# Kernel tuning notes

Measured on AMD Instinct MI355X. Metric: run time of the kernel, lower is better.

## Reference

```python
import jax, jax.numpy as jnp
import numpy as np

N = 50000          # nodes
E = 800000         # edges
F_IN = 128         # node_features
HID = 128          # hidden_dim
OUT = 64           # out_channels
TOP = 4            # top_features (gate channels)
EXP = 3            # experts
G = 64             # num graphs in batch
TEMP = 101.0       # 100 - 0/(200*0.01) + final_temperature(1.0) at batch counter 0


def setup_inputs() -> dict:
    key = jax.random.key(0)
    ks = jax.random.split(key, 12)
    s = 0.08  # weight init scale
    x = jax.random.normal(ks[0], (N, F_IN), jnp.float32)
    top_features = jax.random.normal(ks[1], (N, TOP), jnp.float32)
    edge_index = jax.random.randint(ks[2], (2, E), 0, N, dtype=jnp.int64)
    batch = jnp.sort(jax.random.randint(ks[3], (N,), 0, G, dtype=jnp.int64))
    W0 = jax.random.normal(ks[4], (EXP, F_IN, HID), jnp.float32) * s
    b0 = jax.random.normal(ks[5], (EXP, HID), jnp.float32) * s
    Wg0 = jax.random.normal(ks[6], (EXP, TOP), jnp.float32) * s
    W1 = jax.random.normal(ks[7], (EXP, HID, HID), jnp.float32) * s
    b1 = jax.random.normal(ks[8], (EXP, HID), jnp.float32) * s
    Wg1 = jax.random.normal(ks[9], (EXP, TOP), jnp.float32) * s
    Wf = jax.random.normal(ks[10], (HID, OUT), jnp.float32) * s
    bf = jax.random.normal(ks[11], (OUT,), jnp.float32) * s
    return {"x": x, "top_features": top_features, "edge_index": edge_index,
            "batch": batch, "W0": W0, "b0": b0, "Wg0": Wg0,
            "W1": W1, "b1": b1, "Wg1": Wg1, "Wf": Wf, "bf": bf}


def reference(x, top_features, edge_index, batch, W0, b0, Wg0, W1, b1, Wg1, Wf, bf):
    # GCN with self-loops and symmetric normalization (PyG GCNConv default)
    sl = jnp.arange(N, dtype=edge_index.dtype)
    src = jnp.concatenate([edge_index[0], sl])
    dst = jnp.concatenate([edge_index[1], sl])
    deg = jax.ops.segment_sum(jnp.ones_like(src, jnp.float32), dst, num_segments=N)
    dinv = jax.lax.rsqrt(deg)  # deg >= 1 thanks to self loops
    norm = dinv[src] * dinv[dst]  # [E+N]

    def camoe_layer(h, W, b, Wg):
        # gate: softmax over experts at temperature TEMP
        gate = jax.nn.softmax((top_features @ Wg.T) / TEMP, axis=-1)  # [N, EXP]
        out = jnp.zeros((N, W.shape[2]), h.dtype)
        for e in range(EXP):  # small fixed expert loop (keeps peak memory low)
            he = h @ W[e]                                            # [N, HID]
            agg = jax.ops.segment_sum(he[src] * norm[:, None], dst, num_segments=N)
            out = out + gate[:, e:e + 1] * jax.nn.relu(agg + b[e])
        return out

    h = camoe_layer(x, W0, b0, Wg0)
    # F.dropout before last layer: eval mode -> identity
    h = camoe_layer(h, W1, b1, Wg1)

    # global mean pool over graphs
    sums = jax.ops.segment_sum(h, batch, num_segments=G)             # [G, HID]
    cnt = jax.ops.segment_sum(jnp.ones((N,), h.dtype), batch, num_segments=G)
    pooled = sums / jnp.maximum(cnt, 1.0)[:, None]
    return pooled @ Wf + bf                                          # [G, OUT]
```

## Files before the change

kernel.cpp:

```cpp
#include <hip/hip_runtime.h>
#include <hip/hip_bf16.h>

#define HID 128
#define EXP 3
#define TOP 4
#define OUTC 64
#define SLOTC 64

typedef __bf16 bf16x8 __attribute__((ext_vector_type(8)));
typedef float f32x16 __attribute__((ext_vector_type(16)));
typedef float f32x2 __attribute__((ext_vector_type(2)));

#define GLDS_STRIDE 272
#define OUT_STRIDE 132
#define SLOT_LDS_OFF (64 * GLDS_STRIDE)

__device__ __forceinline__ unsigned int pack4_fp8(float a, float b, float c, float d) {
    int v = 0;
    v = __builtin_amdgcn_cvt_pk_fp8_f32(a, b, v, false);
    v = __builtin_amdgcn_cvt_pk_fp8_f32(c, d, v, true);
    return (unsigned int)v;
}

__device__ __forceinline__ void unpack4_fp8(unsigned int v, float* out) {
    f32x2 lo = __builtin_amdgcn_cvt_pk_f32_fp8((int)v, false);
    f32x2 hi = __builtin_amdgcn_cvt_pk_f32_fp8((int)v, true);
    out[0] = lo[0]; out[1] = lo[1]; out[2] = hi[0]; out[3] = hi[1];
}

__device__ __forceinline__ void add16_fp8(uint4 a, float* acc) {
    unsigned int q[4] = {a.x, a.y, a.z, a.w};
#pragma unroll
    for (int k = 0; k < 4; ++k) {
        float f[4];
        unpack4_fp8(q[k], f);
#pragma unroll
        for (int j = 0; j < 4; ++j) acc[k * 4 + j] += f[j];
    }
}


__global__ __launch_bounds__(256) void mega0_kernel(
        const int* __restrict__ src, const int* __restrict__ dst,
        int* __restrict__ cnt, int* __restrict__ slots, int E,
        const float* __restrict__ tf, const float* __restrict__ Wg0,
        const float* __restrict__ Wg1, float* __restrict__ gates,
        const int* __restrict__ batch, int* __restrict__ gstart,
        const float* __restrict__ W0, const float* __restrict__ W1,
        __bf16* __restrict__ ph0, __bf16* __restrict__ ph1,
        int N, int G, int nFill, int nGate) {
    int b = blockIdx.x;
    int t = threadIdx.x;

    if (b < nFill) {
        int slice = b & 7;
        int base = (b >> 3) * 2048 + t * 8;
        if (base < E) {
            if (base + 8 <= E) {
                int4 d0 = *(const int4*)(dst + base);
                int4 d1 = *(const int4*)(dst + base + 4);
                int dv[8] = {d0.x, d0.y, d0.z, d0.w, d1.x, d1.y, d1.z, d1.w};
#pragma unroll
                for (int k = 0; k < 8; ++k) {
                    int d = dv[k];
                    if (((d >> 6) & 7) != slice) continue;
                    int s = src[base + k];
                    int p = atomicAdd(&cnt[d], 1);
                    if (p < SLOTC) slots[(size_t)d * SLOTC + p] = s;
                }
            } else {
                for (int i = base; i < E; ++i) {
                    int d = dst[i];
                    if (((d >> 6) & 7) != slice) continue;
                    int s = src[i];
                    int p = atomicAdd(&cnt[d], 1);
                    if (p < SLOTC) slots[(size_t)d * SLOTC + p] = s;
                }
            }
        }
        return;
    }
    b -= nFill;
    if (b < nGate) {
        int n = b * 256 + t;
        if (n >= N) return;
        float4 tv = *(const float4*)(tf + (size_t)n * TOP);
        const float* Wg[2] = {Wg0, Wg1};
#pragma unroll
        for (int l = 0; l < 2; ++l) {
            float lg[EXP];
#pragma unroll
            for (int e = 0; e < EXP; ++e) {
                const float* w = Wg[l] + e * TOP;
                lg[e] = (tv.x * w[0] + tv.y * w[1] + tv.z * w[2] + tv.w * w[3]) * (1.0f / 101.0f);
            }
            float m = fmaxf(lg[0], fmaxf(lg[1], lg[2]));
            float e0 = expf(lg[0] - m), e1 = expf(lg[1] - m), e2 = expf(lg[2] - m);
            float inv = 1.0f / (e0 + e1 + e2);
            gates[n * 6 + l * 3 + 0] = e0 * inv;
            gates[n * 6 + l * 3 + 1] = e1 * inv;
            gates[n * 6 + l * 3 + 2] = e2 * inv;
        }
        return;
    }
    b -= nGate;
    if (b == 0) {
        int g = t;
        if (g > G) return;
        if (g == G) { gstart[G] = N; return; }
        int lo = 0, hi = N;
        while (lo < hi) {
            int mid = (lo + hi) >> 1;
            if (batch[mid] < g) lo = mid + 1; else hi = mid;
        }
        gstart[g] = lo;
        return;
    }
    b -= 1;
    int job = b * 4 + (t >> 6);
    if (job >= 192) return;
    int l = t & 63;
    int layer = job / 96;
    int rem = job % 96;
    int e = rem / 32;
    int s = (rem % 32) / 4;
    int c = rem % 4;
    const float* W = layer ? W1 : W0;
    __bf16* ph = layer ? ph1 : ph0;
    size_t dstbase = (size_t)((((e * 8 + s) * 4 + c) * 64 + l)) * 8;
    int kbase = s * 16 + (l >> 5) * 8;
    int ncol = c * 32 + (l & 31);
#pragma unroll
    for (int j = 0; j < 8; ++j) {
        float w = W[(size_t)e * (HID * HID) + (size_t)(kbase + j) * HID + ncol];
        ph[dstbase + j] = (__bf16)w;
    }
}


__global__ __launch_bounds__(256) void prep2_kernel(const float* __restrict__ x,
                                                    unsigned int* __restrict__ x8,
                                                    const int* __restrict__ cnt, int N) {
    int i = blockIdx.x * 256 + threadIdx.x;
    int total16 = N * (HID / 16);
    if (i >= total16) return;
    int n = i >> 3;
    float dn = rsqrtf((float)cnt[n] + 1.0f);
    const float4* xp = (const float4*)x + (size_t)i * 4;
    float4 v0 = xp[0], v1 = xp[1], v2 = xp[2], v3 = xp[3];
    uint4 o;
    o.x = pack4_fp8(v0.x * dn, v0.y * dn, v0.z * dn, v0.w * dn);
    o.y = pack4_fp8(v1.x * dn, v1.y * dn, v1.z * dn, v1.w * dn);
    o.z = pack4_fp8(v2.x * dn, v2.y * dn, v2.z * dn, v2.w * dn);
    o.w = pack4_fp8(v3.x * dn, v3.y * dn, v3.z * dn, v3.w * dn);
    ((uint4*)x8)[i] = o;
}


__global__ __launch_bounds__(512, 4) void fused_layer_kernel(
        const unsigned char* __restrict__ h8in,
        const __bf16* __restrict__ wpkh,
        const float* __restrict__ bias, const float* __restrict__ gates, int gate_off,
        const int* __restrict__ cnt, const int* __restrict__ slots,
        unsigned char* __restrict__ hout8,
        const int* __restrict__ batch, float* __restrict__ pooled, int N) {
    __shared__ char lds[64 * OUT_STRIDE * 4];
    int tid = threadIdx.x;
    int row0 = blockIdx.x * 64;

    {
        uint4* sdst = (uint4*)(lds + SLOT_LDS_OFF);
        const uint4* ssrc = (const uint4*)(slots + (size_t)row0 * SLOTC);
        sdst[tid] = ssrc[tid];
        sdst[tid + 512] = ssrc[tid + 512];
    }
    __syncthreads();

    {
        int r = tid >> 3;
        int part = tid & 7;
        int n = row0 + r;
        float acc[16];
#pragma unroll
        for (int j = 0; j < 16; ++j) acc[j] = 0.f;
        if (n < N) {
            const unsigned char* hb = h8in + part * 16;
            int degt = cnt[n];
            int deg = min(degt, SLOTC);
            float dn = rsqrtf((float)degt + 1.0f);
            uint4 v = *(const uint4*)(hb + (size_t)n * HID);
            {
                unsigned int q[4] = {v.x, v.y, v.z, v.w};
#pragma unroll
                for (int k = 0; k < 4; ++k) {
                    float f[4];
                    unpack4_fp8(q[k], f);
#pragma unroll
                    for (int j = 0; j < 4; ++j) acc[k * 4 + j] = f[j];
                }
            }
            const int* sl = (const int*)(lds + SLOT_LDS_OFF) + r * SLOTC;
            int i = 0;
            for (; i + 4 <= deg; i += 4) {
                int4 sv = *(const int4*)(sl + i);
                uint4 a0 = *(const uint4*)(hb + (size_t)sv.x * HID);
                uint4 a1 = *(const uint4*)(hb + (size_t)sv.y * HID);
                uint4 a2 = *(const uint4*)(hb + (size_t)sv.z * HID);
                uint4 a3 = *(const uint4*)(hb + (size_t)sv.w * HID);
                add16_fp8(a0, acc);
                add16_fp8(a1, acc);
                add16_fp8(a2, acc);
                add16_fp8(a3, acc);
            }
            for (; i < deg; ++i) {
                uint4 a0 = *(const uint4*)(hb + (size_t)sl[i] * HID);
                add16_fp8(a0, acc);
            }
#pragma unroll
            for (int j = 0; j < 16; ++j) acc[j] *= dn;
        }
        char* drow = lds + r * GLDS_STRIDE + part * 32;
        bf16x8 h0, h1;
#pragma unroll
        for (int j = 0; j < 8; ++j) { h0[j] = (__bf16)acc[j]; h1[j] = (__bf16)acc[8 + j]; }
        *(bf16x8*)drow = h0;
        *(bf16x8*)(drow + 16) = h1;
    }
    __syncthreads();

    int lane = tid & 63;
    int wave = tid >> 6;
    int m = lane & 31;
    int g = lane >> 5;
    int rhalf = wave & 1;
    int cq = wave >> 1;
    const char* arow = lds + (rhalf * 32 + m) * GLDS_STRIDE + g * 16;
    int rowbase = row0 + rhalf * 32 + 4 * g;

    float F[16];
#pragma unroll
    for (int r = 0; r < 16; ++r) F[r] = 0.f;

    for (int e = 0; e < EXP; ++e) {
        f32x16 acc;
#pragma unroll
        for (int r = 0; r < 16; ++r) acc[r] = 0.f;

#pragma unroll
        for (int s = 0; s < 8; ++s) {
            bf16x8 Ah = *(const bf16x8*)(arow + s * 32);
            bf16x8 Bh = *(const bf16x8*)(wpkh + (size_t)(((e * 8 + s) * 4 + cq) * 64 + lane) * 8);
            acc = __builtin_amdgcn_mfma_f32_32x32x16_bf16(Ah, Bh, acc, 0, 0, 0);
        }
        float gt[16];
#pragma unroll
        for (int r = 0; r < 16; ++r) {
            int rr = rowbase + (r & 3) + 8 * (r >> 2);
            gt[r] = (rr < N) ? gates[(size_t)rr * 6 + gate_off + e] : 0.f;
        }
        float bb = bias[e * HID + cq * 32 + m];
#pragma unroll
        for (int r = 0; r < 16; ++r)
            F[r] += gt[r] * fmaxf(acc[r] + bb, 0.f);
    }

    __syncthreads();
    float* lds32 = (float*)lds;
    {
        int colg = cq * 32 + m;
#pragma unroll
        for (int r = 0; r < 16; ++r) {
            int lr = rhalf * 32 + 4 * g + (r & 3) + 8 * (r >> 2);
            lds32[lr * OUT_STRIDE + colg] = F[r];
        }
    }
    __syncthreads();

    if (hout8) {
#pragma unroll
        for (int it = 0; it < 4; ++it) {
            int id = tid + it * 512;
            int r = id >> 5;
            int c4 = id & 31;
            int gr = row0 + r;
            if (gr < N) {
                float dr = rsqrtf((float)cnt[gr] + 1.0f);
                const float* src = &lds32[r * OUT_STRIDE + c4 * 4];
                *(unsigned int*)(hout8 + (size_t)gr * HID + c4 * 4) =
                    pack4_fp8(src[0] * dr, src[1] * dr, src[2] * dr, src[3] * dr);
            }
        }
    }
    if (pooled) {
        int col = tid & 127;
        int rbase = (tid >> 7) * 16;
        int cur = -1;
        float acc = 0.f;
        for (int r = 0; r < 16; ++r) {
            int gr = row0 + rbase + r;
            if (gr >= N) break;
            int gb = batch[gr];
            if (gb != cur) {
                if (cur >= 0) atomicAdd(&pooled[cur * HID + col], acc);
                acc = 0.f;
                cur = gb;
            }
            acc += lds32[(rbase + r) * OUT_STRIDE + col];
        }
        if (cur >= 0) atomicAdd(&pooled[cur * HID + col], acc);
    }
}


__global__ __launch_bounds__(64) void final_kernel(const float* __restrict__ pooled,
                                                   const int* __restrict__ gstart,
                                                   const float* __restrict__ Wf,
                                                   const float* __restrict__ bf,
                                                   float* __restrict__ out) {
    __shared__ float ps[HID];
    int g = blockIdx.x;
    int o = threadIdx.x;
    float invc = 1.0f / fmaxf((float)(gstart[g + 1] - gstart[g]), 1.0f);
    ps[o] = pooled[g * HID + o] * invc;
    ps[o + 64] = pooled[g * HID + o + 64] * invc;
    __syncthreads();
    float acc = bf[o];
#pragma unroll 8
    for (int k = 0; k < HID; ++k) acc = fmaf(ps[k], Wf[k * OUTC + o], acc);
    out[g * OUTC + o] = acc;
}


extern "C" void kernel_launch(void* const* d_in, const int* in_sizes, int n_in,
                              void* d_out, int out_size, void* d_ws, size_t ws_size,
                              hipStream_t stream) {
    const float* x   = (const float*)d_in[0];
    const float* tf  = (const float*)d_in[1];
    const int*   ei  = (const int*)d_in[2];
    const int*   bat = (const int*)d_in[3];
    const float* W0  = (const float*)d_in[4];
    const float* b0  = (const float*)d_in[5];
    const float* Wg0 = (const float*)d_in[6];
    const float* W1  = (const float*)d_in[7];
    const float* b1  = (const float*)d_in[8];
    const float* Wg1 = (const float*)d_in[9];
    const float* Wf  = (const float*)d_in[10];
    const float* bf  = (const float*)d_in[11];
    float* out = (float*)d_out;

    const int N = in_sizes[0] / HID;
    const int E = in_sizes[2] / 2;
    const int G = out_size / OUTC;

    char* p = (char*)d_ws;
    auto alloc = [&](size_t bytes) -> void* {
        void* r = (void*)p;
        p += (bytes + 255) & ~(size_t)255;
        return r;
    };
    int*           cnt    = (int*)alloc((size_t)N * 4);
    float*         pooled = (float*)alloc((size_t)G * HID * 4);
    int*           slots  = (int*)alloc((size_t)(N + 64) * SLOTC * 4);
    float*         gates  = (float*)alloc((size_t)N * 6 * 4);
    unsigned char* x8     = (unsigned char*)alloc((size_t)N * HID);
    unsigned char* h8b    = (unsigned char*)alloc((size_t)N * HID);
    int*           gstart = (int*)alloc((size_t)(G + 1) * 4);
    __bf16*        wpkh0  = (__bf16*)alloc((size_t)EXP * HID * HID * 2);
    __bf16*        wpkh1  = (__bf16*)alloc((size_t)EXP * HID * HID * 2);

    const int* src = ei;
    const int* dst = ei + E;

    size_t zlen = (size_t)((char*)pooled - (char*)cnt) + (size_t)G * HID * 4;
    hipMemsetAsync(cnt, 0, zlen, stream);

    const int nFill = ((E + 2047) / 2048) * 8;
    const int nGate = (N + 255) / 256;
    const int megaBlocks = nFill + nGate + 1 + 48;

    mega0_kernel<<<megaBlocks, 256, 0, stream>>>(src, dst, cnt, slots, E,
                                                 tf, Wg0, Wg1, gates,
                                                 bat, gstart,
                                                 W0, W1, wpkh0, wpkh1,
                                                 N, G, nFill, nGate);

    const int prepBlocks = (N * (HID / 16) + 255) / 256;
    prep2_kernel<<<prepBlocks, 256, 0, stream>>>(x, (unsigned int*)x8, cnt, N);

    int gemm_blocks = (N + 63) / 64;

    fused_layer_kernel<<<gemm_blocks, 512, 0, stream>>>(x8, wpkh0, b0, gates, 0,
                                                        cnt, slots,
                                                        h8b, nullptr, nullptr, N);
    fused_layer_kernel<<<gemm_blocks, 512, 0, stream>>>(h8b, wpkh1, b1, gates, 3,
                                                        cnt, slots,
                                                        nullptr, bat, pooled, N);

    final_kernel<<<G, 64, 0, stream>>>(pooled, gstart, Wf, bf, out);
}
```

Baseline: 217.6 us.

## Fold x fp8 conversion into setup kernel and apply source norm in gather

The separate prep kernel, which scaled x by the source degree normalisation before converting to fp8, is removed. The conversion now runs as extra blocks inside the first mega kernel, without scaling, since it no longer has to wait for the degree counts. The first fused layer is templated to apply the per-source rsqrt(deg) weight during aggregation by reading cnt for each neighbour. This removes one launch and one dependency stage, at the cost of extra scattered cnt loads and FMAs in the layer-0 gather. Quantising unscaled x to fp8 also changes rounding behaviour.

```diff
diff --git a/kernel.cpp b/kernel.cpp
--- a/kernel.cpp
+++ b/kernel.cpp
@@ -28,13 +28,24 @@
     out[0] = lo[0]; out[1] = lo[1]; out[2] = hi[0]; out[3] = hi[1];
 }
 
-__device__ __forceinline__ void add16_fp8(uint4 a, float* acc) {
+__device__ __forceinline__ void fma16_fp8(uint4 a, float w, float* acc) {
     unsigned int q[4] = {a.x, a.y, a.z, a.w};
 #pragma unroll
     for (int k = 0; k < 4; ++k) {
         float f[4];
         unpack4_fp8(q[k], f);
 #pragma unroll
+        for (int j = 0; j < 4; ++j) acc[k * 4 + j] += f[j] * w;
+    }
+}
+
+__device__ __forceinline__ void add16_fp8(uint4 a, float* acc) {
+    unsigned int q[4] = {a.x, a.y, a.z, a.w};
+#pragma unroll
+    for (int k = 0; k < 4; ++k) {
+        float f[4];
+        unpack4_fp8(q[k], f);
+#pragma unroll
         for (int j = 0; j < 4; ++j) acc[k * 4 + j] += f[j];
     }
 }
@@ -43,12 +54,13 @@
 __global__ __launch_bounds__(256) void mega0_kernel(
         const int* __restrict__ src, const int* __restrict__ dst,
         int* __restrict__ cnt, int* __restrict__ slots, int E,
+        const float* __restrict__ x, unsigned int* __restrict__ x8,
         const float* __restrict__ tf, const float* __restrict__ Wg0,
         const float* __restrict__ Wg1, float* __restrict__ gates,
         const int* __restrict__ batch, int* __restrict__ gstart,
         const float* __restrict__ W0, const float* __restrict__ W1,
         __bf16* __restrict__ ph0, __bf16* __restrict__ ph1,
-        int N, int G, int nFill, int nGate) {
+        int N, int G, int nFill, int nConv, int nGate) {
     int b = blockIdx.x;
     int t = threadIdx.x;
 
@@ -81,6 +93,22 @@
         return;
     }
     b -= nFill;
+    if (b < nConv) {
+        int i = b * 256 + t;
+        int total16 = N * (HID / 16);
+        if (i < total16) {
+            const float4* xp = (const float4*)x + (size_t)i * 4;
+            float4 v0 = xp[0], v1 = xp[1], v2 = xp[2], v3 = xp[3];
+            uint4 o;
+            o.x = pack4_fp8(v0.x, v0.y, v0.z, v0.w);
+            o.y = pack4_fp8(v1.x, v1.y, v1.z, v1.w);
+            o.z = pack4_fp8(v2.x, v2.y, v2.z, v2.w);
+            o.w = pack4_fp8(v3.x, v3.y, v3.z, v3.w);
+            ((uint4*)x8)[i] = o;
+        }
+        return;
+    }
+    b -= nConv;
     if (b < nGate) {
         int n = b * 256 + t;
         if (n >= N) return;
@@ -138,25 +166,7 @@
 }
 
 
-__global__ __launch_bounds__(256) void prep2_kernel(const float* __restrict__ x,
-                                                    unsigned int* __restrict__ x8,
-                                                    const int* __restrict__ cnt, int N) {
-    int i = blockIdx.x * 256 + threadIdx.x;
-    int total16 = N * (HID / 16);
-    if (i >= total16) return;
-    int n = i >> 3;
-    float dn = rsqrtf((float)cnt[n] + 1.0f);
-    const float4* xp = (const float4*)x + (size_t)i * 4;
-    float4 v0 = xp[0], v1 = xp[1], v2 = xp[2], v3 = xp[3];
-    uint4 o;
-    o.x = pack4_fp8(v0.x * dn, v0.y * dn, v0.z * dn, v0.w * dn);
-    o.y = pack4_fp8(v1.x * dn, v1.y * dn, v1.z * dn, v1.w * dn);
-    o.z = pack4_fp8(v2.x * dn, v2.y * dn, v2.z * dn, v2.w * dn);
-    o.w = pack4_fp8(v3.x * dn, v3.y * dn, v3.z * dn, v3.w * dn);
-    ((uint4*)x8)[i] = o;
-}
-
-
+template <bool WEIGHTED>
 __global__ __launch_bounds__(512, 4) void fused_layer_kernel(
         const unsigned char* __restrict__ h8in,
         const __bf16* __restrict__ wpkh,
@@ -191,12 +201,13 @@
             uint4 v = *(const uint4*)(hb + (size_t)n * HID);
             {
                 unsigned int q[4] = {v.x, v.y, v.z, v.w};
+                float sw = WEIGHTED ? dn : 1.0f;
 #pragma unroll
                 for (int k = 0; k < 4; ++k) {
                     float f[4];
                     unpack4_fp8(q[k], f);
 #pragma unroll
-                    for (int j = 0; j < 4; ++j) acc[k * 4 + j] = f[j];
+                    for (int j = 0; j < 4; ++j) acc[k * 4 + j] = f[j] * sw;
                 }
             }
             const int* sl = (const int*)(lds + SLOT_LDS_OFF) + r * SLOTC;
@@ -207,14 +218,24 @@
                 uint4 a1 = *(const uint4*)(hb + (size_t)sv.y * HID);
                 uint4 a2 = *(const uint4*)(hb + (size_t)sv.z * HID);
                 uint4 a3 = *(const uint4*)(hb + (size_t)sv.w * HID);
-                add16_fp8(a0, acc);
-                add16_fp8(a1, acc);
-                add16_fp8(a2, acc);
-                add16_fp8(a3, acc);
+                if (WEIGHTED) {
+                    int c0 = cnt[sv.x], c1 = cnt[sv.y], c2 = cnt[sv.z], c3 = cnt[sv.w];
+                    fma16_fp8(a0, rsqrtf((float)c0 + 1.0f), acc);
+                    fma16_fp8(a1, rsqrtf((float)c1 + 1.0f), acc);
+                    fma16_fp8(a2, rsqrtf((float)c2 + 1.0f), acc);
+                    fma16_fp8(a3, rsqrtf((float)c3 + 1.0f), acc);
+                } else {
+                    add16_fp8(a0, acc);
+                    add16_fp8(a1, acc);
+                    add16_fp8(a2, acc);
+                    add16_fp8(a3, acc);
+                }
             }
             for (; i < deg; ++i) {
-                uint4 a0 = *(const uint4*)(hb + (size_t)sl[i] * HID);
-                add16_fp8(a0, acc);
+                int s0 = sl[i];
+                uint4 a0 = *(const uint4*)(hb + (size_t)s0 * HID);
+                if (WEIGHTED) fma16_fp8(a0, rsqrtf((float)cnt[s0] + 1.0f), acc);
+                else          add16_fp8(a0, acc);
             }
 #pragma unroll
             for (int j = 0; j < 16; ++j) acc[j] *= dn;
@@ -375,26 +396,25 @@
     hipMemsetAsync(cnt, 0, zlen, stream);
 
     const int nFill = ((E + 2047) / 2048) * 8;
+    const int nConv = (N * (HID / 16) + 255) / 256;
     const int nGate = (N + 255) / 256;
-    const int megaBlocks = nFill + nGate + 1 + 48;
+    const int megaBlocks = nFill + nConv + nGate + 1 + 48;
 
     mega0_kernel<<<megaBlocks, 256, 0, stream>>>(src, dst, cnt, slots, E,
+                                                 x, (unsigned int*)x8,
                                                  tf, Wg0, Wg1, gates,
                                                  bat, gstart,
                                                  W0, W1, wpkh0, wpkh1,
-                                                 N, G, nFill, nGate);
-
-    const int prepBlocks = (N * (HID / 16) + 255) / 256;
-    prep2_kernel<<<prepBlocks, 256, 0, stream>>>(x, (unsigned int*)x8, cnt, N);
+                                                 N, G, nFill, nConv, nGate);
 
     int gemm_blocks = (N + 63) / 64;
 
-    fused_layer_kernel<<<gemm_blocks, 512, 0, stream>>>(x8, wpkh0, b0, gates, 0,
-                                                        cnt, slots,
-                                                        h8b, nullptr, nullptr, N);
-    fused_layer_kernel<<<gemm_blocks, 512, 0, stream>>>(h8b, wpkh1, b1, gates, 3,
-                                                        cnt, slots,
-                                                        nullptr, bat, pooled, N);
+    fused_layer_kernel<true><<<gemm_blocks, 512, 0, stream>>>(x8, wpkh0, b0, gates, 0,
+                                                              cnt, slots,
+                                                              h8b, nullptr, nullptr, N);
+    fused_layer_kernel<false><<<gemm_blocks, 512, 0, stream>>>(h8b, wpkh1, b1, gates, 3,
+                                                               cnt, slots,
+                                                               nullptr, bat, pooled, N);
 
     final_kernel<<<G, 64, 0, stream>>>(pooled, gstart, Wf, bf, out);
 }
```

After: 217.2 us. About the same (-0.2%).
